# Kernel optimization log

Hardware: AMD Instinct MI355X
Metric: run time of the kernel (lower is better)

The kernel has to match this reference:

```python
import jax, jax.numpy as jnp
import numpy as np

# DenseCRFHead hyperparameters (init_kwargs)
WEIGHT = 1e-8
SIGMA_RGB = 15.0
SIGMA_XY = 100.0
SCALE = 0.5


def setup_inputs() -> dict:
    key = jax.random.key(0)
    k1, k2 = jax.random.split(key)
    N, C, H, W = 8, 3, 64, 64          # images already at scaled resolution
    K, Hs, Ws = 21, 128, 128           # segmentations at full resolution
    images = jax.random.uniform(k1, (N, C, H, W), dtype=jnp.float32) * 255.0
    segmentations = jax.random.uniform(k2, (N, K, Hs, Ws), dtype=jnp.float32)
    return {"images": images, "segmentations": segmentations}


def reference(images, segmentations):
    N, K, H2, W2 = segmentations.shape
    H, W = int(H2 * SCALE), int(W2 * SCALE)
    P = H * W

    # F.interpolate(..., scale_factor, mode='bilinear', align_corners=False)
    seg = jax.image.resize(segmentations, (N, K, H, W), method="bilinear")
    segf = seg.reshape(N, K, P)

    # images are not differentiated in the original custom Function (grad None)
    img = jax.lax.stop_gradient(images)

    # bilateral features: spatial scaled by sigma_xy*scale_factor, color by sigma_rgb
    sxy = SIGMA_XY * SCALE
    ys, xs = jnp.meshgrid(jnp.arange(H, dtype=jnp.float32),
                          jnp.arange(W, dtype=jnp.float32), indexing="ij")
    pos = jnp.stack([xs, ys], axis=-1).reshape(P, 2) / sxy          # [P,2]
    col = img.reshape(N, 3, P).transpose(0, 2, 1) / SIGMA_RGB       # [N,P,3]

    d_xy = jnp.sum((pos[:, None, :] - pos[None, :, :]) ** 2, axis=-1)  # [P,P]

    def per_image(args):
        cn, sn = args                                   # [P,3], [K,P]
        d_rgb = jnp.sum((cn[:, None, :] - cn[None, :, :]) ** 2, axis=-1)
        Wk = jnp.exp(-0.5 * (d_xy + d_rgb))             # [P,P] bilateral kernel
        return jnp.einsum("ij,kj->ki", Wk, sn)          # AS = W @ seg

    # sequential over batch keeps peak memory to one [P,P] kernel
    AS = jax.lax.map(per_image, (col, segf))            # [N,K,P]

    loss = -jnp.sum(segf * AS) / N
    return (WEIGHT * loss).reshape(1)
```

## Files before the change

### kernel.cpp

```cpp
#include <hip/hip_runtime.h>

#define NP   4096
#define NIMG 8
#define NK   21
#define ROWH 32
#define NT   16
#define ITEMS_PER_IMG 136
#define N_ITEMS (NIMG * ITEMS_PER_IMG)
#define N_SLOTS (N_ITEMS * 2)

#define FEAT_SCALE 0.84932180028801907f

typedef _Float16 half8 __attribute__((ext_vector_type(8)));
typedef float f32x4 __attribute__((ext_vector_type(4)));

__device__ __forceinline__ unsigned short h2u(_Float16 h) {
  union { _Float16 f; unsigned short u; } c; c.f = h; return c.u;
}

__device__ __forceinline__ void resize_w(int o, float* w, int* t) {
  const float ww[4] = {0.25f, 0.75f, 0.75f, 0.25f};
  float s = 0.f;
  #pragma unroll
  for (int a = 0; a < 4; ++a) {
    int tap = 2 * o - 1 + a;
    bool v = (tap >= 0) && (tap < 128);
    w[a] = v ? ww[a] : 0.f;
    t[a] = v ? tap : 0;
    s += w[a];
  }
  float inv = 1.f / s;
  #pragma unroll
  for (int a = 0; a < 4; ++a) w[a] *= inv;
}

__global__ void __launch_bounds__(256) prep_kernel(const float* __restrict__ images,
                                                   const float* __restrict__ segs,
                                                   _Float16* __restrict__ distA,
                                                   _Float16* __restrict__ distB,
                                                   _Float16* __restrict__ segh) {
  int bid = blockIdx.x;
  int tid = threadIdx.x;
  int n = bid / 112;
  int r112 = bid % 112;
  int oyg = r112 / 7, kq = r112 % 7;
  int ox = tid & 63, oyl = tid >> 6;
  int oy = oyg * 4 + oyl;
  int p = oy * 64 + ox;
  int idx = n * NP + p;

  if (kq == 0) {
    const float cxy  = FEAT_SCALE / 50.0f;
    const float crgb = FEAT_SCALE / 15.0f;
    const float* img = images + (size_t)n * 3 * NP;
    float f[5];
    f[0] = (float)ox * cxy;
    f[1] = (float)oy * cxy;
    f[2] = img[0 * NP + p] * crgb;
    f[3] = img[1 * NP + p] * crgb;
    f[4] = img[2 * NP + p] * crgb;

    _Float16 ah[5], al[5];
    float n2 = 0.f;
    #pragma unroll
    for (int d = 0; d < 5; ++d) {
      ah[d] = (_Float16)f[d];
      float rem = f[d] - (float)ah[d];
      al[d] = (_Float16)rem;
      float at = (float)ah[d] + (float)al[d];
      n2 = fmaf(at, at, n2);
    }
    _Float16 nh = (_Float16)n2;
    _Float16 nl = (_Float16)(n2 - (float)nh);

    _Float16 rowA[ROWH], rowB[ROWH];
    #pragma unroll
    for (int q = 0; q < ROWH; ++q) { rowA[q] = (_Float16)0.f; rowB[q] = (_Float16)0.f; }
    #pragma unroll
    for (int d = 0; d < 5; ++d) {
      rowA[d]      = ah[d];
      rowA[5 + d]  = al[d];
      rowA[10 + d] = ah[d];
      rowB[d]      = (_Float16)2.f * ah[d];
      rowB[5 + d]  = (_Float16)2.f * ah[d];
      rowB[10 + d] = (_Float16)2.f * al[d];
    }
    rowA[15] = nh;  rowA[16] = nl;  rowA[17] = (_Float16)1.f; rowA[18] = (_Float16)1.f;
    rowB[15] = (_Float16)-1.f; rowB[16] = (_Float16)-1.f; rowB[17] = -nh; rowB[18] = -nl;

    half8* oA = (half8*)(distA + (size_t)idx * ROWH);
    half8* oB = (half8*)(distB + (size_t)idx * ROWH);
    #pragma unroll
    for (int q = 0; q < 4; ++q) {
      oA[q] = ((half8*)rowA)[q];
      oB[q] = ((half8*)rowB)[q];
    }
  }

  __shared__ float slab[2][10][128];
  int r0 = 8 * oyg - 1;
  float wy[4], wx[4]; int ty[4], tx[4];
  resize_w(oy, wy, ty);
  resize_w(ox, wx, tx);

  int lofs[5], lrr[5], lcc[5];
  #pragma unroll
  for (int q = 0; q < 5; ++q) {
    int e = tid + q * 256;
    int rr = e >> 7, cc = e & 127;
    int row = r0 + rr;
    row = row < 0 ? 0 : (row > 127 ? 127 : row);
    lofs[q] = row * 128 + cc;
    lrr[q] = rr; lcc[q] = cc;
  }

  const float* sb = segs + (size_t)n * NK * 128 * 128;
  float rg[5];
  {
    const float* sk = sb + (size_t)(kq * 3) * 128 * 128;
    #pragma unroll
    for (int q = 0; q < 5; ++q) rg[q] = sk[lofs[q]];
    #pragma unroll
    for (int q = 0; q < 5; ++q) slab[0][lrr[q]][lcc[q]] = rg[q];
  }

  float outk[3];
  #pragma unroll
  for (int kk = 0; kk < 3; ++kk) {
    if (kk < 2) {
      const float* sk = sb + (size_t)(kq * 3 + kk + 1) * 128 * 128;
      #pragma unroll
      for (int q = 0; q < 5; ++q) rg[q] = sk[lofs[q]];
    }
    __syncthreads();
    float a = 0.f;
    #pragma unroll
    for (int ay = 0; ay < 4; ++ay) {
      int rel = 2 * oyl + ay;
      float rsum = 0.f;
      #pragma unroll
      for (int ax = 0; ax < 4; ++ax) rsum = fmaf(wx[ax], slab[kk & 1][rel][tx[ax]], rsum);
      a = fmaf(wy[ay], rsum, a);
    }
    outk[kk] = a;
    if (kk < 2) {
      #pragma unroll
      for (int q = 0; q < 5; ++q) slab[(kk & 1) ^ 1][lrr[q]][lcc[q]] = rg[q];
    }
  }

  char* rowp = (char*)(segh + (size_t)idx * ROWH);
  #pragma unroll
  for (int kk = 0; kk < 3; ++kk)
    *(unsigned short*)(rowp + 6 * kq + 2 * kk) = h2u((_Float16)outk[kk]);
  if (kq == 6) {
    *(unsigned short*)    (rowp + 42) = 0;
    *(unsigned int*)      (rowp + 44) = 0u;
    *(unsigned long long*)(rowp + 48) = 0ull;
    *(unsigned long long*)(rowp + 56) = 0ull;
  }
}

__global__ void __launch_bounds__(256, 8) crf_mfma(const _Float16* __restrict__ distA,
                                                   const _Float16* __restrict__ distB,
                                                   const _Float16* __restrict__ segh,
                                                   float* __restrict__ slots) {
  __shared__ char lds[16384];
  int bid = blockIdx.x;
  int item = bid >> 1, h = bid & 1;
  int n = item / ITEMS_PER_IMG;
  int rem = item % ITEMS_PER_IMG;
  int I = 0;
  while (rem >= NT - I) { rem -= NT - I; ++I; }
  int J = I + rem;

  int tid = threadIdx.x;
  int lane = tid & 63, wid = tid >> 6;
  int r = lane & 15, g4 = lane >> 4;

  const char* dA = (const char*)(distA + (size_t)n * NP * ROWH);
  const char* dB = (const char*)(distB + (size_t)n * NP * ROWH);
  const char* sg = (const char*)(segh  + (size_t)n * NP * ROWH);

  {
    const char* srcBd = dB + (size_t)(J * 256 + h * 128) * 64;
    const char* srcBs = sg + (size_t)(J * 256 + h * 128) * 64;
    #pragma unroll
    for (int q = 0; q < 2; ++q) {
      int e = tid + q * 256;
      float4 vd = *(const float4*)(srcBd + e * 16);
      float4 vs = *(const float4*)(srcBs + e * 16);
      int dof = (e & 3) * 2048 + (e >> 2) * 16;
      *(float4*)(lds + dof) = vd;
      *(float4*)(lds + 8192 + dof) = vs;
    }
  }

  half8 Ad[4], As[4];
  #pragma unroll
  for (int m = 0; m < 4; ++m) {
    size_t aoff = (size_t)(I * 256 + (wid * 4 + m) * 16 + r) * 64 + g4 * 16;
    Ad[m] = *(const half8*)(dA + aoff);
    As[m] = *(const half8*)(sg + aoff);
  }
  __syncthreads();

  f32x4 zero = {0.f, 0.f, 0.f, 0.f};
  float sm0 = 0.f, sm1 = 0.f, sm2 = 0.f, sm3 = 0.f;
  float sum;

  if (J > I) {
    const char* bp0 = lds + g4 * 2048 + r * 16;
    half8 Bd = *(const half8*)bp0;
    half8 Bs = *(const half8*)(bp0 + 8192);
    #pragma unroll 4
    for (int jt = 0; jt < 8; ++jt) {
      int jn = (jt < 7) ? jt + 1 : jt;
      const char* bp = lds + g4 * 2048 + (jn * 16 + r) * 16;
      half8 nBd = *(const half8*)bp;
      half8 nBs = *(const half8*)(bp + 8192);
      #pragma unroll
      for (int m = 0; m < 4; ++m) {
        f32x4 ad  = __builtin_amdgcn_mfma_f32_16x16x32_f16(Ad[m], Bd, zero, 0, 0, 0);
        f32x4 as_ = __builtin_amdgcn_mfma_f32_16x16x32_f16(As[m], Bs, zero, 0, 0, 0);
        float t0 = fmaf(__builtin_amdgcn_exp2f(ad[0]), as_[0],
                   fmaf(__builtin_amdgcn_exp2f(ad[1]), as_[1], 0.f));
        float t1 = fmaf(__builtin_amdgcn_exp2f(ad[2]), as_[2],
                   fmaf(__builtin_amdgcn_exp2f(ad[3]), as_[3], 0.f));
        float t = t0 + t1;
        if (m == 0) sm0 += t; else if (m == 1) sm1 += t;
        else if (m == 2) sm2 += t; else sm3 += t;
      }
      Bd = nBd; Bs = nBs;
    }
    sum = 2.f * (sm0 + sm1 + sm2 + sm3);
  } else {
    #pragma unroll 2
    for (int jt = 0; jt < 8; ++jt) {
      int jta = I * 16 + h * 8 + jt;
      const char* bp = lds + g4 * 2048 + (jt * 16 + r) * 16;
      half8 Bd = *(const half8*)bp;
      half8 Bs = *(const half8*)(bp + 8192);
      #pragma unroll
      for (int m = 0; m < 4; ++m) {
        int it = I * 16 + wid * 4 + m;
        if (jta >= it) {
          float s = (jta > it) ? 2.f : 1.f;
          f32x4 ad  = __builtin_amdgcn_mfma_f32_16x16x32_f16(Ad[m], Bd, zero, 0, 0, 0);
          f32x4 as_ = __builtin_amdgcn_mfma_f32_16x16x32_f16(As[m], Bs, zero, 0, 0, 0);
          float t0 = fmaf(__builtin_amdgcn_exp2f(ad[0]), as_[0],
                     fmaf(__builtin_amdgcn_exp2f(ad[1]), as_[1], 0.f));
          float t1 = fmaf(__builtin_amdgcn_exp2f(ad[2]), as_[2],
                     fmaf(__builtin_amdgcn_exp2f(ad[3]), as_[3], 0.f));
          float t = s * (t0 + t1);
          if (m == 0) sm0 += t; else if (m == 1) sm1 += t;
          else if (m == 2) sm2 += t; else sm3 += t;
        }
      }
    }
    sum = sm0 + sm1 + sm2 + sm3;
  }

  #pragma unroll
  for (int off = 32; off > 0; off >>= 1) sum += __shfl_down(sum, off);
  __syncthreads();
  float* red = (float*)lds;
  if (lane == 0) red[wid] = sum;
  __syncthreads();
  if (tid == 0) slots[bid] = red[0] + red[1] + red[2] + red[3];
}

__global__ void __launch_bounds__(256) reduce_kernel(const float* __restrict__ slots,
                                                     float* __restrict__ out) {
  __shared__ double dred[4];
  int tid = threadIdx.x;
  int lane = tid & 63, wid = tid >> 6;
  double s = 0.0;
  #pragma unroll
  for (int q = 0; q < 9; ++q) {
    int k = tid + q * 256;
    if (k < N_SLOTS) s += (double)slots[k];
  }
  #pragma unroll
  for (int off = 32; off > 0; off >>= 1) s += __shfl_down(s, off);
  if (lane == 0) dred[wid] = s;
  __syncthreads();
  if (tid == 0) {
    double tot = dred[0] + dred[1] + dred[2] + dred[3];
    out[0] = (float)(tot * (-1e-8 / 8.0));
  }
}

extern "C" void kernel_launch(void* const* d_in, const int* in_sizes, int n_in,
                              void* d_out, int out_size, void* d_ws, size_t ws_size,
                              hipStream_t stream) {
  const float* images = (const float*)d_in[0];
  const float* segs   = (const float*)d_in[1];
  float* out  = (float*)d_out;
  float* slots = (float*)d_ws;
  _Float16* distA = (_Float16*)((char*)d_ws + 16384);
  _Float16* distB = distA + (size_t)NIMG * NP * ROWH;
  _Float16* segh  = distB + (size_t)NIMG * NP * ROWH;

  hipLaunchKernelGGL(prep_kernel, dim3(NIMG * 16 * 7), dim3(256), 0, stream,
                     images, segs, distA, distB, segh);
  hipLaunchKernelGGL(crf_mfma, dim3(N_SLOTS), dim3(256), 0, stream,
                     distA, distB, segh, slots);
  hipLaunchKernelGGL(reduce_kernel, dim3(1), dim3(256), 0, stream, slots, out);
}
```

Measured before the change: 38.73 us.

## Make MFMA kernel persistent with double-buffered LDS prefetch of next item

```diff
diff --git a/kernel.cpp b/kernel.cpp
--- a/kernel.cpp
+++ b/kernel.cpp
@@ -6,8 +6,11 @@
 #define ROWH 32
 #define NT   16
 #define ITEMS_PER_IMG 136
-#define N_ITEMS (NIMG * ITEMS_PER_IMG)
-#define N_SLOTS (N_ITEMS * 2)
+#define N_HALF (NIMG * ITEMS_PER_IMG * 2)
+#define GRID2 1024
+#define GSTRIDE 2064
+#define ASTRIDE 8256
+#define BUFSTRIDE 16512
 
 #define FEAT_SCALE 0.84932180028801907f
 
@@ -161,111 +164,150 @@
   }
 }
 
-__global__ void __launch_bounds__(256, 8) crf_mfma(const _Float16* __restrict__ distA,
+__device__ __forceinline__ void decode_item(int item, int& n, int& I, int& J, int& h) {
+  h = item & 1;
+  int pr = item >> 1;
+  n = pr / ITEMS_PER_IMG;
+  int rem = pr - n * ITEMS_PER_IMG;
+  int I_ = 0;
+  while (rem >= NT - I_) { rem -= NT - I_; ++I_; }
+  I = I_;
+  J = I_ + rem;
+}
+
+__global__ void __launch_bounds__(256, 4) crf_mfma(const _Float16* __restrict__ distA,
                                                    const _Float16* __restrict__ distB,
                                                    const _Float16* __restrict__ segh,
                                                    float* __restrict__ slots) {
-  __shared__ char lds[16384];
+  __shared__ char lds[2 * BUFSTRIDE];
+  __shared__ float red[4];
   int bid = blockIdx.x;
-  int item = bid >> 1, h = bid & 1;
-  int n = item / ITEMS_PER_IMG;
-  int rem = item % ITEMS_PER_IMG;
-  int I = 0;
-  while (rem >= NT - I) { rem -= NT - I; ++I; }
-  int J = I + rem;
-
   int tid = threadIdx.x;
   int lane = tid & 63, wid = tid >> 6;
   int r = lane & 15, g4 = lane >> 4;
 
-  const char* dA = (const char*)(distA + (size_t)n * NP * ROWH);
-  const char* dB = (const char*)(distB + (size_t)n * NP * ROWH);
-  const char* sg = (const char*)(segh  + (size_t)n * NP * ROWH);
-
+  int item = bid;
+  int n, I, J, h;
+  decode_item(item, n, I, J, h);
+
+  float4 rd0, rd1, rs0, rs1;
   {
-    const char* srcBd = dB + (size_t)(J * 256 + h * 128) * 64;
-    const char* srcBs = sg + (size_t)(J * 256 + h * 128) * 64;
-    #pragma unroll
-    for (int q = 0; q < 2; ++q) {
-      int e = tid + q * 256;
-      float4 vd = *(const float4*)(srcBd + e * 16);
-      float4 vs = *(const float4*)(srcBs + e * 16);
-      int dof = (e & 3) * 2048 + (e >> 2) * 16;
-      *(float4*)(lds + dof) = vd;
-      *(float4*)(lds + 8192 + dof) = vs;
-    }
-  }
-
-  half8 Ad[4], As[4];
-  #pragma unroll
-  for (int m = 0; m < 4; ++m) {
-    size_t aoff = (size_t)(I * 256 + (wid * 4 + m) * 16 + r) * 64 + g4 * 16;
-    Ad[m] = *(const half8*)(dA + aoff);
-    As[m] = *(const half8*)(sg + aoff);
-  }
-  __syncthreads();
-
+    const char* srcBd = (const char*)(distB + (size_t)n * NP * ROWH) + (size_t)(J * 256 + h * 128) * 64;
+    const char* srcBs = (const char*)(segh  + (size_t)n * NP * ROWH) + (size_t)(J * 256 + h * 128) * 64;
+    rd0 = *(const float4*)(srcBd + tid * 16);
+    rd1 = *(const float4*)(srcBd + tid * 16 + 4096);
+    rs0 = *(const float4*)(srcBs + tid * 16);
+    rs1 = *(const float4*)(srcBs + tid * 16 + 4096);
+  }
+  {
+    int e0 = tid, e1 = tid + 256;
+    int d0 = (e0 & 3) * GSTRIDE + (e0 >> 2) * 16;
+    int d1 = (e1 & 3) * GSTRIDE + (e1 >> 2) * 16;
+    *(float4*)(lds + d0) = rd0;
+    *(float4*)(lds + d1) = rd1;
+    *(float4*)(lds + ASTRIDE + d0) = rs0;
+    *(float4*)(lds + ASTRIDE + d1) = rs1;
+  }
+
+  float blocksum = 0.f;
+  int cur = 0;
   f32x4 zero = {0.f, 0.f, 0.f, 0.f};
-  float sm0 = 0.f, sm1 = 0.f, sm2 = 0.f, sm3 = 0.f;
-  float sum;
-
-  if (J > I) {
-    const char* bp0 = lds + g4 * 2048 + r * 16;
-    half8 Bd = *(const half8*)bp0;
-    half8 Bs = *(const half8*)(bp0 + 8192);
-    #pragma unroll 4
-    for (int jt = 0; jt < 8; ++jt) {
-      int jn = (jt < 7) ? jt + 1 : jt;
-      const char* bp = lds + g4 * 2048 + (jn * 16 + r) * 16;
-      half8 nBd = *(const half8*)bp;
-      half8 nBs = *(const half8*)(bp + 8192);
-      #pragma unroll
-      for (int m = 0; m < 4; ++m) {
-        f32x4 ad  = __builtin_amdgcn_mfma_f32_16x16x32_f16(Ad[m], Bd, zero, 0, 0, 0);
-        f32x4 as_ = __builtin_amdgcn_mfma_f32_16x16x32_f16(As[m], Bs, zero, 0, 0, 0);
-        float t0 = fmaf(__builtin_amdgcn_exp2f(ad[0]), as_[0],
-                   fmaf(__builtin_amdgcn_exp2f(ad[1]), as_[1], 0.f));
-        float t1 = fmaf(__builtin_amdgcn_exp2f(ad[2]), as_[2],
-                   fmaf(__builtin_amdgcn_exp2f(ad[3]), as_[3], 0.f));
-        float t = t0 + t1;
-        if (m == 0) sm0 += t; else if (m == 1) sm1 += t;
-        else if (m == 2) sm2 += t; else sm3 += t;
-      }
-      Bd = nBd; Bs = nBs;
-    }
-    sum = 2.f * (sm0 + sm1 + sm2 + sm3);
-  } else {
-    #pragma unroll 2
-    for (int jt = 0; jt < 8; ++jt) {
-      int jta = I * 16 + h * 8 + jt;
-      const char* bp = lds + g4 * 2048 + (jt * 16 + r) * 16;
-      half8 Bd = *(const half8*)bp;
-      half8 Bs = *(const half8*)(bp + 8192);
-      #pragma unroll
-      for (int m = 0; m < 4; ++m) {
-        int it = I * 16 + wid * 4 + m;
-        if (jta >= it) {
-          float s = (jta > it) ? 2.f : 1.f;
+
+  #pragma unroll 1
+  for (;;) {
+    int nxt = item + GRID2;
+    bool more = (nxt < N_HALF);
+    int nn = 0, nI = 0, nJ = 0, nh = 0;
+
+    const char* dAn = (const char*)(distA + (size_t)n * NP * ROWH);
+    const char* sgn = (const char*)(segh  + (size_t)n * NP * ROWH);
+    half8 Ad[4], As[4];
+    #pragma unroll
+    for (int m = 0; m < 4; ++m) {
+      size_t aoff = (size_t)(I * 256 + (wid * 4 + m) * 16 + r) * 64 + g4 * 16;
+      Ad[m] = *(const half8*)(dAn + aoff);
+      As[m] = *(const half8*)(sgn + aoff);
+    }
+
+    if (more) {
+      decode_item(nxt, nn, nI, nJ, nh);
+      const char* srcBd = (const char*)(distB + (size_t)nn * NP * ROWH) + (size_t)(nJ * 256 + nh * 128) * 64;
+      const char* srcBs = (const char*)(segh  + (size_t)nn * NP * ROWH) + (size_t)(nJ * 256 + nh * 128) * 64;
+      rd0 = *(const float4*)(srcBd + tid * 16);
+      rd1 = *(const float4*)(srcBd + tid * 16 + 4096);
+      rs0 = *(const float4*)(srcBs + tid * 16);
+      rs1 = *(const float4*)(srcBs + tid * 16 + 4096);
+    }
+
+    __syncthreads();
+
+    const char* buf = lds + cur * BUFSTRIDE;
+    float sm0 = 0.f, sm1 = 0.f, sm2 = 0.f, sm3 = 0.f;
+
+    if (J > I) {
+      #pragma unroll 4
+      for (int jt = 0; jt < 8; ++jt) {
+        const char* bp = buf + g4 * GSTRIDE + (jt * 16 + r) * 16;
+        half8 Bd = *(const half8*)bp;
+        half8 Bs = *(const half8*)(bp + ASTRIDE);
+        #pragma unroll
+        for (int m = 0; m < 4; ++m) {
           f32x4 ad  = __builtin_amdgcn_mfma_f32_16x16x32_f16(Ad[m], Bd, zero, 0, 0, 0);
           f32x4 as_ = __builtin_amdgcn_mfma_f32_16x16x32_f16(As[m], Bs, zero, 0, 0, 0);
           float t0 = fmaf(__builtin_amdgcn_exp2f(ad[0]), as_[0],
                      fmaf(__builtin_amdgcn_exp2f(ad[1]), as_[1], 0.f));
           float t1 = fmaf(__builtin_amdgcn_exp2f(ad[2]), as_[2],
                      fmaf(__builtin_amdgcn_exp2f(ad[3]), as_[3], 0.f));
-          float t = s * (t0 + t1);
+          float t = 2.f * (t0 + t1);
           if (m == 0) sm0 += t; else if (m == 1) sm1 += t;
           else if (m == 2) sm2 += t; else sm3 += t;
         }
       }
-    }
-    sum = sm0 + sm1 + sm2 + sm3;
-  }
-
-  #pragma unroll
-  for (int off = 32; off > 0; off >>= 1) sum += __shfl_down(sum, off);
-  __syncthreads();
-  float* red = (float*)lds;
-  if (lane == 0) red[wid] = sum;
+    } else {
+      #pragma unroll 2
+      for (int jt = 0; jt < 8; ++jt) {
+        int jta = I * 16 + h * 8 + jt;
+        const char* bp = buf + g4 * GSTRIDE + (jt * 16 + r) * 16;
+        half8 Bd = *(const half8*)bp;
+        half8 Bs = *(const half8*)(bp + ASTRIDE);
+        #pragma unroll
+        for (int m = 0; m < 4; ++m) {
+          int it = I * 16 + wid * 4 + m;
+          if (jta >= it) {
+            float s = (jta > it) ? 2.f : 1.f;
+            f32x4 ad  = __builtin_amdgcn_mfma_f32_16x16x32_f16(Ad[m], Bd, zero, 0, 0, 0);
+            f32x4 as_ = __builtin_amdgcn_mfma_f32_16x16x32_f16(As[m], Bs, zero, 0, 0, 0);
+            float t0 = fmaf(__builtin_amdgcn_exp2f(ad[0]), as_[0],
+                       fmaf(__builtin_amdgcn_exp2f(ad[1]), as_[1], 0.f));
+            float t1 = fmaf(__builtin_amdgcn_exp2f(ad[2]), as_[2],
+                       fmaf(__builtin_amdgcn_exp2f(ad[3]), as_[3], 0.f));
+            float t = s * (t0 + t1);
+            if (m == 0) sm0 += t; else if (m == 1) sm1 += t;
+            else if (m == 2) sm2 += t; else sm3 += t;
+          }
+        }
+      }
+    }
+    blocksum += sm0 + sm1 + sm2 + sm3;
+
+    if (!more) break;
+
+    {
+      char* nbuf = lds + (cur ^ 1) * BUFSTRIDE;
+      int e0 = tid, e1 = tid + 256;
+      int d0 = (e0 & 3) * GSTRIDE + (e0 >> 2) * 16;
+      int d1 = (e1 & 3) * GSTRIDE + (e1 >> 2) * 16;
+      *(float4*)(nbuf + d0) = rd0;
+      *(float4*)(nbuf + d1) = rd1;
+      *(float4*)(nbuf + ASTRIDE + d0) = rs0;
+      *(float4*)(nbuf + ASTRIDE + d1) = rs1;
+    }
+    item = nxt; n = nn; I = nI; J = nJ; h = nh; cur ^= 1;
+  }
+
+  #pragma unroll
+  for (int off = 32; off > 0; off >>= 1) blocksum += __shfl_down(blocksum, off);
+  if (lane == 0) red[wid] = blocksum;
   __syncthreads();
   if (tid == 0) slots[bid] = red[0] + red[1] + red[2] + red[3];
 }
@@ -277,10 +319,7 @@
   int lane = tid & 63, wid = tid >> 6;
   double s = 0.0;
   #pragma unroll
-  for (int q = 0; q < 9; ++q) {
-    int k = tid + q * 256;
-    if (k < N_SLOTS) s += (double)slots[k];
-  }
+  for (int q = 0; q < 4; ++q) s += (double)slots[tid + q * 256];
   #pragma unroll
   for (int off = 32; off > 0; off >>= 1) s += __shfl_down(s, off);
   if (lane == 0) dred[wid] = s;
@@ -304,7 +343,7 @@
 
   hipLaunchKernelGGL(prep_kernel, dim3(NIMG * 16 * 7), dim3(256), 0, stream,
                      images, segs, distA, distB, segh);
-  hipLaunchKernelGGL(crf_mfma, dim3(N_SLOTS), dim3(256), 0, stream,
+  hipLaunchKernelGGL(crf_mfma, dim3(GRID2), dim3(256), 0, stream,
                      distA, distB, segh, slots);
   hipLaunchKernelGGL(reduce_kernel, dim3(1), dim3(256), 0, stream, slots, out);
 }
```

After: 33.14 us. -14.4%, faster.
